# Performance work log

Hardware: AMD Instinct MI355X
Metric: run time of the kernel (lower is better)

Reference implementation:

```python
import jax, jax.numpy as jnp
import numpy as np

B, C, H, W, P, D, NH = 16, 3, 512, 512, 16, 128, 4
GH, GW = H // P, W // P
NP_ = GH * GW            # 1024 total patches
PD = C * P * P           # 768 patch dim
NV = NP_ // 4            # 256 visible tokens (mask_ratio = 0.75)
ENC_L, DEC_L = 6, 2
FF = 4 * D

def layer_norm(x, w, b, eps=1e-5):
    m = jnp.mean(x, -1, keepdims=True)
    v = jnp.mean((x - m) ** 2, -1, keepdims=True)
    return (x - m) * jax.lax.rsqrt(v + eps) * w + b

def mha(x, qkv_w, qkv_b, out_w, out_b):
    Bq, S, Dm = x.shape
    hd = Dm // NH
    q, k, v = jnp.split(x @ qkv_w.T + qkv_b, 3, axis=-1)
    sh = lambda t: t.reshape(Bq, S, NH, hd).transpose(0, 2, 1, 3)
    q, k, v = sh(q), sh(k), sh(v)
    scale = jnp.asarray(1.0 / np.sqrt(hd), x.dtype)
    att = jax.nn.softmax(jnp.einsum('bhqd,bhkd->bhqk', q, k) * scale, axis=-1)
    o = jnp.einsum('bhqk,bhkd->bhqd', att, v).transpose(0, 2, 1, 3).reshape(Bq, S, Dm)
    return o @ out_w.T + out_b

def stack(x, qkv_w, qkv_b, out_w, out_b, ln1_w, ln1_b, ff1_w, ff1_b, ff2_w, ff2_b, ln2_w, ln2_b):
    # post-norm nn.TransformerEncoderLayer, eval mode (dropout off), exact gelu
    for i in range(qkv_w.shape[0]):
        x = layer_norm(x + mha(x, qkv_w[i], qkv_b[i], out_w[i], out_b[i]), ln1_w[i], ln1_b[i])
        h = jax.nn.gelu(x @ ff1_w[i].T + ff1_b[i], approximate=False) @ ff2_w[i].T + ff2_b[i]
        x = layer_norm(x + h, ln2_w[i], ln2_b[i])
    return x

def setup_inputs():
    key = jax.random.key(0)
    ks = iter(jax.random.split(key, 64))
    f = lambda *s: jax.random.normal(next(ks), s, jnp.float32) * 0.02
    inp = {
        'x': jax.random.normal(next(ks), (B, C, H, W), jnp.float32),
        'vis_idx': jax.vmap(lambda k: jax.random.permutation(k, NP_))(jax.random.split(next(ks), B))[:, :NV].astype(jnp.int32),
        'w_patch': f(D, PD), 'b_patch': jnp.zeros((D,), jnp.float32),
        'mask_token': f(1, D), 'pos_embed': f(1, NP_, D),
        'w_recon': f(PD, D), 'b_recon': jnp.zeros((PD,), jnp.float32),
    }
    for pre, L in (('enc', ENC_L), ('dec', DEC_L)):
        inp[pre + '_qkv_w'] = f(L, 3 * D, D)
        inp[pre + '_qkv_b'] = jnp.zeros((L, 3 * D), jnp.float32)
        inp[pre + '_out_w'] = f(L, D, D)
        inp[pre + '_out_b'] = jnp.zeros((L, D), jnp.float32)
        inp[pre + '_ln1_w'] = jnp.ones((L, D), jnp.float32)
        inp[pre + '_ln1_b'] = jnp.zeros((L, D), jnp.float32)
        inp[pre + '_ff1_w'] = f(L, FF, D)
        inp[pre + '_ff1_b'] = jnp.zeros((L, FF), jnp.float32)
        inp[pre + '_ff2_w'] = f(L, D, FF)
        inp[pre + '_ff2_b'] = jnp.zeros((L, D), jnp.float32)
        inp[pre + '_ln2_w'] = jnp.ones((L, D), jnp.float32)
        inp[pre + '_ln2_b'] = jnp.zeros((L, D), jnp.float32)
    return inp

def reference(x, vis_idx, w_patch, b_patch, mask_token, pos_embed, w_recon, b_recon,
              enc_qkv_w, enc_qkv_b, enc_out_w, enc_out_b, enc_ln1_w, enc_ln1_b,
              enc_ff1_w, enc_ff1_b, enc_ff2_w, enc_ff2_b, enc_ln2_w, enc_ln2_b,
              dec_qkv_w, dec_qkv_b, dec_out_w, dec_out_b, dec_ln1_w, dec_ln1_b,
              dec_ff1_w, dec_ff1_b, dec_ff2_w, dec_ff2_b, dec_ln2_w, dec_ln2_b):
    # patchify: matches nn.Unfold(kernel=stride=P) channel-major patch layout
    patches = x.reshape(B, C, GH, P, GW, P).transpose(0, 2, 4, 1, 3, 5).reshape(B, NP_, PD)
    tok = patches @ w_patch.T + b_patch                    # [B, NP, D]
    bidx = jnp.arange(B)[:, None]
    vis = tok[bidx, vis_idx]                               # [B, NV, D] packed visible tokens
    enc = stack(vis, enc_qkv_w, enc_qkv_b, enc_out_w, enc_out_b, enc_ln1_w, enc_ln1_b,
                enc_ff1_w, enc_ff1_b, enc_ff2_w, enc_ff2_b, enc_ln2_w, enc_ln2_b)
    # mask_token everywhere, scatter encoded tokens back to their positions
    full = jnp.broadcast_to(mask_token, (B, NP_, D)).at[bidx, vis_idx].set(enc)
    full = full + pos_embed
    dec = stack(full, dec_qkv_w, dec_qkv_b, dec_out_w, dec_out_b, dec_ln1_w, dec_ln1_b,
                dec_ff1_w, dec_ff1_b, dec_ff2_w, dec_ff2_b, dec_ln2_w, dec_ln2_b)
    rec = dec @ w_recon.T + b_recon                        # [B, NP, PD]
    # unpatchify: [B,GH,GW,C,P,P] -> permute(0,3,1,4,2,5) -> [B,C,H,W]
    img = rec.reshape(B, GH, GW, C, P, P).transpose(0, 3, 1, 4, 2, 5).reshape(B, C, H, W)
    return img
```

## Files before the change

kernel.cpp:

```cpp
#include <hip/hip_runtime.h>
#include <math.h>

typedef unsigned short ushort_t;
typedef __attribute__((ext_vector_type(8))) short bf16x8;
typedef __attribute__((ext_vector_type(4))) float f32x4;
typedef __attribute__((ext_vector_type(16))) float f32x16;
typedef __attribute__((ext_vector_type(2))) unsigned uint2v;

__device__ __forceinline__ ushort_t f2bf(float f){
  union{float f; unsigned u;} v; v.f = f;
  unsigned r = v.u + 0x7FFFu + ((v.u >> 16) & 1u);
  return (ushort_t)(r >> 16);
}
__device__ __forceinline__ float bf2f(ushort_t h){
  union{unsigned u; float f;} v; v.u = ((unsigned)h) << 16; return v.f;
}
__device__ __forceinline__ float gelu_exact(float v){
  return 0.5f * v * (1.f + erff(v * 0.70710678118654752f));
}
#define GLD16(gp, lp) __builtin_amdgcn_global_load_lds( \
    (const __attribute__((address_space(1))) void*)(gp), \
    (__attribute__((address_space(3))) void*)(lp), 16, 0, 0)

static __device__ __forceinline__ f32x4 mfma16(bf16x8 a, bf16x8 b, f32x4 c){
  return __builtin_amdgcn_mfma_f32_16x16x32_bf16(a, b, c, 0, 0, 0);
}
static __device__ __forceinline__ f32x16 mfma32(bf16x8 a, bf16x8 b, f32x16 c){
  return __builtin_amdgcn_mfma_f32_32x32x16_bf16(a, b, c, 0, 0, 0);
}

template<int BT, int MI, int SRC, int EPI>
__global__ __launch_bounds__(256) void mfma_gemm(
    const ushort_t* __restrict__ A, const ushort_t* __restrict__ W,
    const float* __restrict__ bias, void* __restrict__ Cout,
    int M, int N, int K, ushort_t* __restrict__ vT, int slog, float qs)
{
  __shared__ ushort_t smem[BT*64 + BT*64];
  ushort_t* Al = smem;
  ushort_t* Wl = smem + BT*64;
  const int tid = threadIdx.x;
  const int lane = tid & 63, w = tid >> 6;
  const int wr = w >> 1, wc = w & 1;
  const int g = lane >> 4, lq = lane & 15;
  const int m0 = blockIdx.y * BT, n0 = blockIdx.x * BT;

  const f32x4 zf = {0.f, 0.f, 0.f, 0.f};
  f32x4 acc[MI][MI];
#pragma unroll
  for (int i = 0; i < MI; ++i)
#pragma unroll
    for (int j = 0; j < MI; ++j) acc[i][j] = zf;

  float bv[MI];
#pragma unroll
  for (int ni = 0; ni < MI; ++ni) bv[ni] = bias[n0 + wc*(BT/2) + ni*16 + lq];

  const int KT = K >> 6;
  for (int kt = 0; kt < KT; ++kt) {
    if (kt) __syncthreads();
    const int k0 = kt << 6;
#pragma unroll
    for (int i = 0; i < BT/32; ++i) {
      int chunk = i*256 + tid;
      int row = chunk >> 3, c = chunk & 7;
      int kk = k0 + ((c ^ (row & 7)) << 3);
      const ushort_t* src;
      if (SRC == 0) {
        src = A + (size_t)(m0 + row) * K + kk;
      } else {
        int gm = m0 + row;
        int bb = gm >> 10, pp = gm & 1023, gh = pp >> 5, gw = pp & 31;
        int ci = kk >> 8, rem = kk & 255, py = rem >> 4, px = rem & 15;
        src = A + ((size_t)((bb*3 + ci)*512 + gh*16 + py) * 512 + gw*16 + px);
      }
      GLD16(src, (char*)Al + chunk*16);
    }
#pragma unroll
    for (int i = 0; i < BT/32; ++i) {
      int chunk = i*256 + tid;
      int row = chunk >> 3, c = chunk & 7;
      int kk = k0 + ((c ^ (row & 7)) << 3);
      GLD16(W + (size_t)(n0 + row) * K + kk, (char*)Wl + chunk*16);
    }
    __syncthreads();
#pragma unroll
    for (int ks = 0; ks < 2; ++ks) {
      bf16x8 af[MI], bfr[MI];
#pragma unroll
      for (int mi = 0; mi < MI; ++mi) {
        int row = wr*(BT/2) + mi*16 + lq;
        int c = (ks*4 + g) ^ (row & 7);
        af[mi] = *(const bf16x8*)((const char*)Al + row*128 + c*16);
      }
#pragma unroll
      for (int ni = 0; ni < MI; ++ni) {
        int row = wc*(BT/2) + ni*16 + lq;
        int c = (ks*4 + g) ^ (row & 7);
        bfr[ni] = *(const bf16x8*)((const char*)Wl + row*128 + c*16);
      }
#pragma unroll
      for (int mi = 0; mi < MI; ++mi)
#pragma unroll
        for (int ni = 0; ni < MI; ++ni)
          acc[mi][ni] = mfma16(af[mi], bfr[ni], acc[mi][ni]);
    }
  }

  if (EPI == 3 && n0 >= 256) {
    const int Sm1 = (1 << slog) - 1;
#pragma unroll
    for (int mi = 0; mi < MI; ++mi) {
      int gm0 = m0 + wr*(BT/2) + mi*16 + g*4;
      int bb = gm0 >> slog, s0 = gm0 & Sm1;
#pragma unroll
      for (int ni = 0; ni < MI; ++ni) {
        int n = n0 + wc*(BT/2) + ni*16 + lq;
        int vcol = n - 256, hh = vcol >> 5, dd = vcol & 31;
        unsigned pw0 = ((unsigned)f2bf(acc[mi][ni][0] + bv[ni])) |
                       (((unsigned)f2bf(acc[mi][ni][1] + bv[ni])) << 16);
        unsigned pw1 = ((unsigned)f2bf(acc[mi][ni][2] + bv[ni])) |
                       (((unsigned)f2bf(acc[mi][ni][3] + bv[ni])) << 16);
        uint2 pk; pk.x = pw0; pk.y = pw1;
        *(uint2*)(vT + (((size_t)(bb*4 + hh)*32 + dd) << slog) + s0) = pk;
      }
    }
    return;
  }

  if (EPI == 2) {
    float* img = (float*)Cout;
#pragma unroll
    for (int mi = 0; mi < MI; ++mi) {
#pragma unroll
      for (int r = 0; r < 4; ++r) {
        int gm = m0 + wr*(BT/2) + mi*16 + g*4 + r;
        int bb = gm >> 10, pp = gm & 1023, gh = pp >> 5, gw = pp & 31;
#pragma unroll
        for (int ni = 0; ni < MI; ++ni) {
          int n = n0 + wc*(BT/2) + ni*16 + lq;
          int ci = n >> 8, rem = n & 255, py = rem >> 4, px = rem & 15;
          img[(size_t)((bb*3 + ci)*512 + gh*16 + py)*512 + gw*16 + px] =
              acc[mi][ni][r] + bv[ni];
        }
      }
    }
  } else {
    const float cs = (EPI == 3 && n0 < 128) ? qs : 1.0f;
    __syncthreads();
    constexpr int CPR = BT/8;
#pragma unroll
    for (int mi = 0; mi < MI; ++mi)
#pragma unroll
      for (int ni = 0; ni < MI; ++ni)
#pragma unroll
        for (int r = 0; r < 4; ++r) {
          int row = wr*(BT/2) + mi*16 + g*4 + r;
          int col = wc*(BT/2) + ni*16 + lq;
          float v = acc[mi][ni][r] + bv[ni];
          if (EPI == 1) v = gelu_exact(v);
          if (EPI == 3) v *= cs;
          int cc = (col >> 3) ^ (row & (CPR-1));
          smem[row*BT + cc*8 + (col & 7)] = f2bf(v);
        }
    __syncthreads();
    ushort_t* Co = (ushort_t*)Cout;
#pragma unroll
    for (int i = 0; i < BT*BT/2048; ++i) {
      int chunk = i*256 + tid;
      int row = chunk / CPR, cc = chunk % CPR;
      int c = cc ^ (row & (CPR-1));
      bf16x8 v = *(const bf16x8*)((const char*)smem + chunk*16);
      *(bf16x8*)(Co + (size_t)(m0+row)*N + n0 + c*8) = v;
    }
  }
}

template<int S, int JS>
__global__ __launch_bounds__(256) void attn32(
    const ushort_t* __restrict__ qkv, const ushort_t* __restrict__ vTg,
    ushort_t* __restrict__ o)
{
  constexpr int LDSB = (JS == 1) ? 16384 : 32768;
  __shared__ __align__(16) char smem[LDSB];
  const int tid = threadIdx.x, lane = tid & 63, w = tid >> 6;
  const int hi = lane >> 5, lq = lane & 31;
  int lin = blockIdx.x;
  int nid = (lin & 7) * 64 + (lin >> 3);
  int bx = nid & 7, bh = nid >> 3;
  int h = bh & 3, b = bh >> 2;
  const int q0 = (JS == 1) ? (bx*128 + w*32) : (bx*32);

  bf16x8 bq0 = *(const bf16x8*)(qkv + (size_t)(b*S + q0 + lq)*384 + h*32 + hi*8);
  bf16x8 bq1 = *(const bf16x8*)(qkv + (size_t)(b*S + q0 + lq)*384 + h*32 + 16 + hi*8);

  f32x16 O;
#pragma unroll
  for (int i = 0; i < 16; ++i) O[i] = 0.f;
  const f32x16 z16 = O;
  float l = 0.f;

  auto stageK = [&](char* Kb, int j0, int ci){
    int k = ci >> 2, cp = ci & 3, c = cp ^ (k & 3);
    GLD16(qkv + (size_t)(b*S + j0 + k)*384 + 128 + h*32 + c*8, Kb + ci*16);
  };
  auto stageV = [&](char* Vb, int j0, int ci){
    int d = ci >> 3, cp = ci & 7, c = cp ^ (d & 7);
    GLD16(vTg + (size_t)(bh*32 + d)*S + j0 + c*8, Vb + ci*16);
  };

  auto sm_pack = [&](const f32x16& stv, unsigned* wd){
    float p[16];
#pragma unroll
    for (int r = 0; r < 16; ++r) { p[r] = __expf(stv[r]); l += p[r]; }
#pragma unroll
    for (int i = 0; i < 8; ++i) {
      unsigned u0 = __float_as_uint(p[2*i])   + 0x8000u;
      unsigned u1 = __float_as_uint(p[2*i+1]) + 0x8000u;
      wd[i] = (u0 >> 16) | (u1 & 0xFFFF0000u);
    }
  };
  auto pvstep = [&](unsigned* wd, const char* Vb, int mt){
    uint2v s02 = __builtin_amdgcn_permlane32_swap(wd[0], wd[2], false, false);
    uint2v s13 = __builtin_amdgcn_permlane32_swap(wd[1], wd[3], false, false);
    uint2v s46 = __builtin_amdgcn_permlane32_swap(wd[4], wd[6], false, false);
    uint2v s57 = __builtin_amdgcn_permlane32_swap(wd[5], wd[7], false, false);
    union { unsigned u[4]; bf16x8 v; } pa0, pa1;
    pa0.u[0] = s02[0]; pa0.u[1] = s13[0]; pa0.u[2] = s02[1]; pa0.u[3] = s13[1];
    pa1.u[0] = s46[0]; pa1.u[1] = s57[0]; pa1.u[2] = s46[1]; pa1.u[3] = s57[1];
    int d = lq;
    bf16x8 v0 = *(const bf16x8*)(Vb + d*128 + (((mt*4 + hi)     ^ (d & 7)) << 4));
    bf16x8 v1 = *(const bf16x8*)(Vb + d*128 + (((mt*4 + 2 + hi) ^ (d & 7)) << 4));
    O = mfma32(pa0.v, v0, O);
    O = mfma32(pa1.v, v1, O);
  };
  auto computeTile = [&](const char* Kb, const char* Vb){
    const int k0 = lq, k1 = 32 + lq;
    bf16x8 a00 = *(const bf16x8*)(Kb + k0*64 + (((hi)     ^ (k0 & 3)) << 4));
    bf16x8 a01 = *(const bf16x8*)(Kb + k0*64 + (((2 + hi) ^ (k0 & 3)) << 4));
    f32x16 st0 = mfma32(a00, bq0, z16);
    st0 = mfma32(a01, bq1, st0);
    bf16x8 a10 = *(const bf16x8*)(Kb + k1*64 + (((hi)     ^ (k1 & 3)) << 4));
    bf16x8 a11 = *(const bf16x8*)(Kb + k1*64 + (((2 + hi) ^ (k1 & 3)) << 4));
    f32x16 st1 = mfma32(a10, bq0, z16);
    st1 = mfma32(a11, bq1, st1);
    unsigned wd0[8], wd1[8];
    sm_pack(st0, wd0);
    sm_pack(st1, wd1);
    pvstep(wd0, Vb, 0);
    pvstep(wd1, Vb, 1);
  };

  if (JS == 4) {
    char* Kb = smem + w*8192;
    char* Vb = Kb + 4096;
    const int j0 = w*64;
#pragma unroll
    for (int i = 0; i < 4; ++i) stageK(Kb, j0, i*64 + lane);
#pragma unroll
    for (int i = 0; i < 4; ++i) stageV(Vb, j0, i*64 + lane);
    __syncthreads();
    computeTile(Kb, Vb);
    float lw = l + __shfl_xor(l, 32);
    __syncthreads();
    float* F = (float*)smem;
#pragma unroll
    for (int r = 0; r < 16; ++r) F[(w*16 + r)*64 + lane] = O[r];
    if (hi == 0) F[4096 + w*32 + lq] = lw;
    __syncthreads();
    if (w == 0) {
      float lt = F[4096 + lq] + F[4096 + 32 + lq] + F[4096 + 64 + lq] + F[4096 + 96 + lq];
      float linv = 1.f / lt;
#pragma unroll
      for (int r = 0; r < 16; ++r) {
        float s = F[r*64 + lane] + F[(16 + r)*64 + lane] +
                  F[(32 + r)*64 + lane] + F[(48 + r)*64 + lane];
        int qr = (r & 3) + 8*(r >> 2) + 4*hi;
        float li = __shfl(linv, qr);
        o[(size_t)(b*S + q0 + qr)*128 + h*32 + lq] = f2bf(s*li);
      }
    }
  } else {
    char* K0 = smem, *V0 = smem + 4096, *K1 = smem + 8192, *V1 = smem + 12288;
    stageK(K0, 0, tid);
    stageV(V0, 0, tid);
    const int NT = S/64;
    for (int t = 0; t < NT; ++t) {
      __syncthreads();
      if (t + 1 < NT) {
        char* Kb = (t & 1) ? K0 : K1;
        char* Vb = (t & 1) ? V0 : V1;
        stageK(Kb, (t + 1)*64, tid);
        stageV(Vb, (t + 1)*64, tid);
      }
      computeTile((t & 1) ? K1 : K0, (t & 1) ? V1 : V0);
    }
    float ltot = l + __shfl_xor(l, 32);
    float linv = 1.f / ltot;
#pragma unroll
    for (int r = 0; r < 16; ++r) {
      int qr = (r & 3) + 8*(r >> 2) + 4*hi;
      float li = __shfl(linv, qr);
      o[(size_t)(b*S + q0 + qr)*128 + h*32 + lq] = f2bf(O[r]*li);
    }
  }
}

__global__ __launch_bounds__(256) void addln_bf16(
    ushort_t* __restrict__ X, const ushort_t* __restrict__ Dl,
    const float* __restrict__ wt, const float* __restrict__ bs)
{
  const int wv = threadIdx.x >> 6, lane = threadIdx.x & 63;
  const size_t row = (size_t)blockIdx.x * 4 + wv;
  ushort_t* xr = X + row*128;
  const ushort_t* dr = Dl + row*128;
  float x1 = bf2f(xr[lane])    + bf2f(dr[lane]);
  float x2 = bf2f(xr[lane+64]) + bf2f(dr[lane+64]);
  float ssum = x1 + x2;
#pragma unroll
  for (int off = 32; off; off >>= 1) ssum += __shfl_xor(ssum, off);
  float mean = ssum * 0.0078125f;
  float d1 = x1 - mean, d2 = x2 - mean;
  float v = d1*d1 + d2*d2;
#pragma unroll
  for (int off = 32; off; off >>= 1) v += __shfl_xor(v, off);
  float rs = rsqrtf(v * 0.0078125f + 1e-5f);
  xr[lane]    = f2bf(d1*rs*wt[lane]    + bs[lane]);
  xr[lane+64] = f2bf(d2*rs*wt[lane+64] + bs[lane+64]);
}

struct CastArgs {
  const float* src[11];
  ushort_t* dst[11];
  int start[11];
};
__global__ __launch_bounds__(256) void cast_all(CastArgs a, int total8){
  int i = blockIdx.x*256 + threadIdx.x;
  if (i >= total8) return;
  int s = 0;
#pragma unroll
  for (int k = 1; k < 11; ++k) if (i >= a.start[k]) s = k;
  int off = (i - a.start[s]) * 8;
  const float* sp = a.src[s] + off;
  float4 f0 = *(const float4*)sp;
  float4 f1 = *(const float4*)(sp + 4);
  bf16x8 r;
  r[0]=(short)f2bf(f0.x); r[1]=(short)f2bf(f0.y); r[2]=(short)f2bf(f0.z); r[3]=(short)f2bf(f0.w);
  r[4]=(short)f2bf(f1.x); r[5]=(short)f2bf(f1.y); r[6]=(short)f2bf(f1.z); r[7]=(short)f2bf(f1.w);
  *(bf16x8*)(a.dst[s] + off) = r;
}

__global__ __launch_bounds__(256) void gather_k(const ushort_t* __restrict__ tok,
    const int* __restrict__ vis, ushort_t* __restrict__ xe){
  int i = blockIdx.x*256 + threadIdx.x;
  int r = i >> 4, e = (i & 15)*8;
  int b = r >> 8;
  int p = vis[r];
  *(bf16x8*)(xe + (size_t)r*128 + e) = *(const bf16x8*)(tok + ((size_t)b*1024 + p)*128 + e);
}

__global__ __launch_bounds__(256) void fill_k(const float* __restrict__ mask_tok,
    const float* __restrict__ pos, ushort_t* __restrict__ full){
  int i = blockIdx.x*256 + threadIdx.x;
  int off0 = i*8;
  int d = off0 & 127;
  int p = (off0 >> 7) & 1023;
  float4 m0 = *(const float4*)(mask_tok + d);
  float4 m1 = *(const float4*)(mask_tok + d + 4);
  const float* pp = pos + (size_t)p*128 + d;
  float4 p0 = *(const float4*)pp, p1 = *(const float4*)(pp + 4);
  bf16x8 r;
  r[0]=(short)f2bf(m0.x+p0.x); r[1]=(short)f2bf(m0.y+p0.y);
  r[2]=(short)f2bf(m0.z+p0.z); r[3]=(short)f2bf(m0.w+p0.w);
  r[4]=(short)f2bf(m1.x+p1.x); r[5]=(short)f2bf(m1.y+p1.y);
  r[6]=(short)f2bf(m1.z+p1.z); r[7]=(short)f2bf(m1.w+p1.w);
  *(bf16x8*)(full + off0) = r;
}

__global__ __launch_bounds__(256) void scatter_k(const ushort_t* __restrict__ enc,
    const int* __restrict__ vis, const float* __restrict__ pos, ushort_t* __restrict__ full){
  int i = blockIdx.x*256 + threadIdx.x;
  int r = i >> 4, e = (i & 15)*8;
  int b = r >> 8;
  int p = vis[r];
  bf16x8 ev = *(const bf16x8*)(enc + (size_t)r*128 + e);
  const float* pp = pos + (size_t)p*128 + e;
  float4 p0 = *(const float4*)pp, p1 = *(const float4*)(pp + 4);
  bf16x8 out;
  out[0]=(short)f2bf(bf2f((ushort_t)ev[0]) + p0.x);
  out[1]=(short)f2bf(bf2f((ushort_t)ev[1]) + p0.y);
  out[2]=(short)f2bf(bf2f((ushort_t)ev[2]) + p0.z);
  out[3]=(short)f2bf(bf2f((ushort_t)ev[3]) + p0.w);
  out[4]=(short)f2bf(bf2f((ushort_t)ev[4]) + p1.x);
  out[5]=(short)f2bf(bf2f((ushort_t)ev[5]) + p1.y);
  out[6]=(short)f2bf(bf2f((ushort_t)ev[6]) + p1.z);
  out[7]=(short)f2bf(bf2f((ushort_t)ev[7]) + p1.w);
  *(bf16x8*)(full + ((size_t)b*1024 + p)*128 + e) = out;
}

extern "C" void kernel_launch(void* const* d_in, const int* in_sizes, int n_in,
                              void* d_out, int out_size, void* d_ws, size_t ws_size,
                              hipStream_t stream)
{
  const float* x        = (const float*)d_in[0];
  const int*   vis      = (const int*)d_in[1];
  const float* b_patch  = (const float*)d_in[3];
  const float* mask_tok = (const float*)d_in[4];
  const float* pos      = (const float*)d_in[5];
  const float* b_recon  = (const float*)d_in[7];
  float* out = (float*)d_out;
  const float QS = 0.17677669529663687f;

  ushort_t* ws    = (ushort_t*)d_ws;
  ushort_t* tok   = ws;
  ushort_t* xe    = tok  + 2097152;
  ushort_t* qkvb  = xe   + 524288;
  ushort_t* obuf  = qkvb + 8388608;
  ushort_t* tbuf  = obuf + 2097152;
  ushort_t* xbf   = tbuf + 2097152;
  ushort_t* wbf   = xbf  + 12582912;

  ushort_t* w_qkv_e = wbf;
  ushort_t* w_out_e = w_qkv_e + 294912;
  ushort_t* w_ff1_e = w_out_e + 98304;
  ushort_t* w_ff2_e = w_ff1_e + 393216;
  ushort_t* w_qkv_d = w_ff2_e + 393216;
  ushort_t* w_out_d = w_qkv_d + 98304;
  ushort_t* w_ff1_d = w_out_d + 32768;
  ushort_t* w_ff2_d = w_ff1_d + 131072;
  ushort_t* w_pat   = w_ff2_d + 131072;
  ushort_t* w_rec   = w_pat   + 98304;
  ushort_t* vT      = w_rec   + 98304;

  CastArgs ca;
  const float* srcs[11] = {x, (const float*)d_in[8], (const float*)d_in[10],
                           (const float*)d_in[14], (const float*)d_in[16],
                           (const float*)d_in[20], (const float*)d_in[22],
                           (const float*)d_in[26], (const float*)d_in[28],
                           (const float*)d_in[2], (const float*)d_in[6]};
  ushort_t* dsts[11] = {xbf, w_qkv_e, w_out_e, w_ff1_e, w_ff2_e,
                        w_qkv_d, w_out_d, w_ff1_d, w_ff2_d, w_pat, w_rec};
  int sizes[11] = {12582912, 294912, 98304, 393216, 393216,
                   98304, 32768, 131072, 131072, 98304, 98304};
  int acc8 = 0;
  for (int k = 0; k < 11; ++k){ ca.src[k]=srcs[k]; ca.dst[k]=dsts[k]; ca.start[k]=acc8; acc8 += sizes[k]/8; }
  cast_all<<<dim3((acc8 + 255)/256), 256, 0, stream>>>(ca, acc8);

  mfma_gemm<64,2,1,0><<<dim3(2,256), 256, 0, stream>>>(xbf, w_pat, b_patch, tok, 16384, 128, 768, nullptr, 0, 1.f);
  gather_k<<<dim3(256), 256, 0, stream>>>(tok, vis, xe);

  for (int L = 0; L < 6; ++L) {
    const float* qb  = (const float*)d_in[9]  + L*384;
    const float* ob  = (const float*)d_in[11] + L*128;
    const float* l1w = (const float*)d_in[12] + L*128;
    const float* l1b = (const float*)d_in[13] + L*128;
    const float* f1b = (const float*)d_in[15] + L*512;
    const float* f2b = (const float*)d_in[17] + L*128;
    const float* l2w = (const float*)d_in[18] + L*128;
    const float* l2b = (const float*)d_in[19] + L*128;
    mfma_gemm<64,2,0,3><<<dim3(6,64), 256, 0, stream>>>(xe, w_qkv_e + L*49152, qb, qkvb, 4096, 384, 128, vT, 8, QS);
    attn32<256,4><<<dim3(512), 256, 0, stream>>>(qkvb, vT, obuf);
    mfma_gemm<64,2,0,0><<<dim3(2,64), 256, 0, stream>>>(obuf, w_out_e + L*16384, ob, tbuf, 4096, 128, 128, nullptr, 0, 1.f);
    addln_bf16<<<dim3(1024), 256, 0, stream>>>(xe, tbuf, l1w, l1b);
    mfma_gemm<64,2,0,1><<<dim3(8,64), 256, 0, stream>>>(xe, w_ff1_e + L*65536, f1b, qkvb, 4096, 512, 128, nullptr, 0, 1.f);
    mfma_gemm<64,2,0,0><<<dim3(2,64), 256, 0, stream>>>(qkvb, w_ff2_e + L*65536, f2b, tbuf, 4096, 128, 512, nullptr, 0, 1.f);
    addln_bf16<<<dim3(1024), 256, 0, stream>>>(xe, tbuf, l2w, l2b);
  }

  fill_k<<<dim3(1024), 256, 0, stream>>>(mask_tok, pos, tok);
  scatter_k<<<dim3(256), 256, 0, stream>>>(xe, vis, pos, tok);

  for (int L = 0; L < 2; ++L) {
    const float* qb  = (const float*)d_in[21] + L*384;
    const float* ob  = (const float*)d_in[23] + L*128;
    const float* l1w = (const float*)d_in[24] + L*128;
    const float* l1b = (const float*)d_in[25] + L*128;
    const float* f1b = (const float*)d_in[27] + L*512;
    const float* f2b = (const float*)d_in[29] + L*128;
    const float* l2w = (const float*)d_in[30] + L*128;
    const float* l2b = (const float*)d_in[31] + L*128;
    mfma_gemm<128,4,0,3><<<dim3(3,128), 256, 0, stream>>>(tok, w_qkv_d + L*49152, qb, qkvb, 16384, 384, 128, vT, 10, QS);
    attn32<1024,1><<<dim3(512), 256, 0, stream>>>(qkvb, vT, obuf);
    mfma_gemm<64,2,0,0><<<dim3(2,256), 256, 0, stream>>>(obuf, w_out_d + L*16384, ob, tbuf, 16384, 128, 128, nullptr, 0, 1.f);
    addln_bf16<<<dim3(4096), 256, 0, stream>>>(tok, tbuf, l1w, l1b);
    mfma_gemm<128,4,0,1><<<dim3(4,128), 256, 0, stream>>>(tok, w_ff1_d + L*65536, f1b, qkvb, 16384, 512, 128, nullptr, 0, 1.f);
    mfma_gemm<64,2,0,0><<<dim3(2,256), 256, 0, stream>>>(qkvb, w_ff2_d + L*65536, f2b, tbuf, 16384, 128, 512, nullptr, 0, 1.f);
    addln_bf16<<<dim3(4096), 256, 0, stream>>>(tok, tbuf, l2w, l2b);
  }

  mfma_gemm<128,4,0,2><<<dim3(6,128), 256, 0, stream>>>(tok, w_rec, b_recon, out, 16384, 768, 128, nullptr, 0, 1.f);
}
```

Before: 396.8 us.

## Fuse out-proj with residual LayerNorm and whole FFN with residual LayerNorm

Replaces the out-projection GEMM plus separate add+LayerNorm with one gemm_ln kernel that adds bias and residual and normalizes in the epilogue, using a cross-wave reduction through shared memory. It also replaces FF1 GEMM, FF2 GEMM and add+LayerNorm with one ffn_ln kernel that keeps the 32x512 GELU hidden tile in LDS. This removes the round trips of the hidden activation and temporary buffers through global memory and cuts several launches per layer. In exchange the blocks are small (32 rows), so only 128 or 512 blocks are launched, every block reloads all of W1/W2 from global memory, there is no double buffering, and variance is computed as E[x^2]-mean^2.

New measurement: 400.1 us. About the same (+0.8%).

```diff
diff --git a/kernel.cpp b/kernel.cpp
--- a/kernel.cpp
+++ b/kernel.cpp
@@ -157,7 +157,6 @@
           int row = wr*(BT/2) + mi*16 + g*4 + r;
           int col = wc*(BT/2) + ni*16 + lq;
           float v = acc[mi][ni][r] + bv[ni];
-          if (EPI == 1) v = gelu_exact(v);
           if (EPI == 3) v *= cs;
           int cc = (col >> 3) ^ (row & (CPR-1));
           smem[row*BT + cc*8 + (col & 7)] = f2bf(v);
@@ -173,6 +172,245 @@
       *(bf16x8*)(Co + (size_t)(m0+row)*N + n0 + c*8) = v;
     }
   }
+}
+
+template<int KK>
+__global__ __launch_bounds__(256) void gemm_ln(
+    const ushort_t* __restrict__ A, const ushort_t* __restrict__ W,
+    const float* __restrict__ bias, ushort_t* __restrict__ X,
+    const float* __restrict__ lnw, const float* __restrict__ lnb)
+{
+  __shared__ __align__(16) ushort_t Al[32*64];
+  __shared__ __align__(16) ushort_t Wl[128*64];
+  __shared__ float red[2][32][4];
+  const int tid = threadIdx.x, lane = tid & 63, w = tid >> 6;
+  const int g = lane >> 4, lq = lane & 15;
+  const int m0 = blockIdx.x * 32;
+  const f32x4 zf = {0.f,0.f,0.f,0.f};
+  f32x4 acc[2][2] = {{zf,zf},{zf,zf}};
+
+#pragma unroll
+  for (int kt = 0; kt < KK/64; ++kt) {
+    if (kt) __syncthreads();
+    const int k0 = kt*64;
+    { int row = tid >> 3, c = tid & 7;
+      int kk = k0 + ((c ^ (row & 7)) << 3);
+      GLD16(A + (size_t)(m0+row)*KK + kk, (char*)Al + tid*16); }
+#pragma unroll
+    for (int i = 0; i < 4; ++i) {
+      int chunk = i*256 + tid, row = chunk >> 3, c = chunk & 7;
+      int kk = k0 + ((c ^ (row & 7)) << 3);
+      GLD16(W + (size_t)row*KK + kk, (char*)Wl + chunk*16);
+    }
+    __syncthreads();
+#pragma unroll
+    for (int ks = 0; ks < 2; ++ks) {
+      bf16x8 af[2], bfr[2];
+#pragma unroll
+      for (int mi = 0; mi < 2; ++mi) {
+        int row = mi*16 + lq, c = (ks*4 + g) ^ (row & 7);
+        af[mi] = *(const bf16x8*)((const char*)Al + row*128 + c*16);
+      }
+#pragma unroll
+      for (int ni = 0; ni < 2; ++ni) {
+        int row = w*32 + ni*16 + lq, c = (ks*4 + g) ^ (row & 7);
+        bfr[ni] = *(const bf16x8*)((const char*)Wl + row*128 + c*16);
+      }
+#pragma unroll
+      for (int mi = 0; mi < 2; ++mi)
+#pragma unroll
+        for (int ni = 0; ni < 2; ++ni)
+          acc[mi][ni] = mfma16(af[mi], bfr[ni], acc[mi][ni]);
+    }
+  }
+
+  float bv[2], lwv[2], lbv[2];
+#pragma unroll
+  for (int ni = 0; ni < 2; ++ni) {
+    int col = w*32 + ni*16 + lq;
+    bv[ni] = bias[col]; lwv[ni] = lnw[col]; lbv[ni] = lnb[col];
+  }
+  float v[2][2][4];
+#pragma unroll
+  for (int mi = 0; mi < 2; ++mi)
+#pragma unroll
+    for (int r = 0; r < 4; ++r) {
+      int row = m0 + mi*16 + g*4 + r;
+#pragma unroll
+      for (int ni = 0; ni < 2; ++ni) {
+        int col = w*32 + ni*16 + lq;
+        v[mi][ni][r] = acc[mi][ni][r] + bv[ni] + bf2f(X[(size_t)row*128 + col]);
+      }
+      float s = v[mi][0][r] + v[mi][1][r];
+      float q = v[mi][0][r]*v[mi][0][r] + v[mi][1][r]*v[mi][1][r];
+      s += __shfl_xor(s,1); s += __shfl_xor(s,2); s += __shfl_xor(s,4); s += __shfl_xor(s,8);
+      q += __shfl_xor(q,1); q += __shfl_xor(q,2); q += __shfl_xor(q,4); q += __shfl_xor(q,8);
+      if (lq == 0) { red[0][mi*16+g*4+r][w] = s; red[1][mi*16+g*4+r][w] = q; }
+    }
+  __syncthreads();
+#pragma unroll
+  for (int mi = 0; mi < 2; ++mi)
+#pragma unroll
+    for (int r = 0; r < 4; ++r) {
+      int rl = mi*16 + g*4 + r;
+      float s = red[0][rl][0]+red[0][rl][1]+red[0][rl][2]+red[0][rl][3];
+      float q = red[1][rl][0]+red[1][rl][1]+red[1][rl][2]+red[1][rl][3];
+      float mean = s * 0.0078125f;
+      float var = q * 0.0078125f - mean*mean;
+      float rstd = rsqrtf(var + 1e-5f);
+#pragma unroll
+      for (int ni = 0; ni < 2; ++ni) {
+        int col = w*32 + ni*16 + lq;
+        X[(size_t)(m0+rl)*128 + col] = f2bf((v[mi][ni][r]-mean)*rstd*lwv[ni] + lbv[ni]);
+      }
+    }
+}
+
+__global__ __launch_bounds__(256) void ffn_ln(
+    ushort_t* __restrict__ X,
+    const ushort_t* __restrict__ W1, const float* __restrict__ b1,
+    const ushort_t* __restrict__ W2, const float* __restrict__ b2,
+    const float* __restrict__ lnw, const float* __restrict__ lnb)
+{
+  __shared__ __align__(16) ushort_t Xl[2*32*64];
+  __shared__ __align__(16) ushort_t Hl[8*32*64];
+  __shared__ __align__(16) ushort_t Wl[128*64];
+  __shared__ float red[2][32][4];
+  const int tid = threadIdx.x, lane = tid & 63, w = tid >> 6;
+  const int g = lane >> 4, lq = lane & 15;
+  const int m0 = blockIdx.x * 32;
+  const f32x4 zf = {0.f,0.f,0.f,0.f};
+
+#pragma unroll
+  for (int i = 0; i < 2; ++i) {
+    int chunk = i*256 + tid;
+    int kt = chunk >> 8, r8 = chunk & 255, row = r8 >> 3, c = r8 & 7;
+    int kk = kt*64 + ((c ^ (row & 7)) << 3);
+    GLD16(X + (size_t)(m0+row)*128 + kk, (char*)Xl + chunk*16);
+  }
+
+#pragma unroll
+  for (int hp = 0; hp < 4; ++hp) {
+    f32x4 acc1[2][2] = {{zf,zf},{zf,zf}};
+#pragma unroll
+    for (int kt = 0; kt < 2; ++kt) {
+      __syncthreads();
+#pragma unroll
+      for (int i = 0; i < 4; ++i) {
+        int chunk = i*256 + tid, row = chunk >> 3, c = chunk & 7;
+        int kk = kt*64 + ((c ^ (row & 7)) << 3);
+        GLD16(W1 + (size_t)(hp*128 + row)*128 + kk, (char*)Wl + chunk*16);
+      }
+      __syncthreads();
+#pragma unroll
+      for (int ks = 0; ks < 2; ++ks) {
+        bf16x8 af[2], bfr[2];
+#pragma unroll
+        for (int mi = 0; mi < 2; ++mi) {
+          int row = mi*16 + lq, c = (ks*4 + g) ^ (row & 7);
+          af[mi] = *(const bf16x8*)((const char*)Xl + kt*4096 + row*128 + c*16);
+        }
+#pragma unroll
+        for (int ni = 0; ni < 2; ++ni) {
+          int row = w*32 + ni*16 + lq, c = (ks*4 + g) ^ (row & 7);
+          bfr[ni] = *(const bf16x8*)((const char*)Wl + row*128 + c*16);
+        }
+#pragma unroll
+        for (int mi = 0; mi < 2; ++mi)
+#pragma unroll
+          for (int ni = 0; ni < 2; ++ni)
+            acc1[mi][ni] = mfma16(af[mi], bfr[ni], acc1[mi][ni]);
+      }
+    }
+#pragma unroll
+    for (int ni = 0; ni < 2; ++ni) {
+      int hid = hp*128 + w*32 + ni*16 + lq;
+      float bb = b1[hid];
+      int hkt = hid >> 6, hc = (hid & 63) >> 3, he = hid & 7;
+#pragma unroll
+      for (int mi = 0; mi < 2; ++mi)
+#pragma unroll
+        for (int r = 0; r < 4; ++r) {
+          int mrow = mi*16 + g*4 + r;
+          float hv = gelu_exact(acc1[mi][ni][r] + bb);
+          *(ushort_t*)((char*)Hl + hkt*4096 + mrow*128 +
+                       ((hc ^ (mrow & 7)) << 4) + he*2) = f2bf(hv);
+        }
+    }
+  }
+
+  f32x4 acc2[2][2] = {{zf,zf},{zf,zf}};
+#pragma unroll
+  for (int kt = 0; kt < 8; ++kt) {
+    __syncthreads();
+#pragma unroll
+    for (int i = 0; i < 4; ++i) {
+      int chunk = i*256 + tid, row = chunk >> 3, c = chunk & 7;
+      int kk = kt*64 + ((c ^ (row & 7)) << 3);
+      GLD16(W2 + (size_t)row*512 + kk, (char*)Wl + chunk*16);
+    }
+    __syncthreads();
+#pragma unroll
+    for (int ks = 0; ks < 2; ++ks) {
+      bf16x8 af[2], bfr[2];
+#pragma unroll
+      for (int mi = 0; mi < 2; ++mi) {
+        int row = mi*16 + lq, c = (ks*4 + g) ^ (row & 7);
+        af[mi] = *(const bf16x8*)((const char*)Hl + kt*4096 + row*128 + c*16);
+      }
+#pragma unroll
+      for (int ni = 0; ni < 2; ++ni) {
+        int row = w*32 + ni*16 + lq, c = (ks*4 + g) ^ (row & 7);
+        bfr[ni] = *(const bf16x8*)((const char*)Wl + row*128 + c*16);
+      }
+#pragma unroll
+      for (int mi = 0; mi < 2; ++mi)
+#pragma unroll
+        for (int ni = 0; ni < 2; ++ni)
+          acc2[mi][ni] = mfma16(af[mi], bfr[ni], acc2[mi][ni]);
+    }
+  }
+
+  float bv[2], lwv[2], lbv[2];
+#pragma unroll
+  for (int ni = 0; ni < 2; ++ni) {
+    int col = w*32 + ni*16 + lq;
+    bv[ni] = b2[col]; lwv[ni] = lnw[col]; lbv[ni] = lnb[col];
+  }
+  float v[2][2][4];
+#pragma unroll
+  for (int mi = 0; mi < 2; ++mi)
+#pragma unroll
+    for (int r = 0; r < 4; ++r) {
+      int row = m0 + mi*16 + g*4 + r;
+#pragma unroll
+      for (int ni = 0; ni < 2; ++ni) {
+        int col = w*32 + ni*16 + lq;
+        v[mi][ni][r] = acc2[mi][ni][r] + bv[ni] + bf2f(X[(size_t)row*128 + col]);
+      }
+      float s = v[mi][0][r] + v[mi][1][r];
+      float q = v[mi][0][r]*v[mi][0][r] + v[mi][1][r]*v[mi][1][r];
+      s += __shfl_xor(s,1); s += __shfl_xor(s,2); s += __shfl_xor(s,4); s += __shfl_xor(s,8);
+      q += __shfl_xor(q,1); q += __shfl_xor(q,2); q += __shfl_xor(q,4); q += __shfl_xor(q,8);
+      if (lq == 0) { red[0][mi*16+g*4+r][w] = s; red[1][mi*16+g*4+r][w] = q; }
+    }
+  __syncthreads();
+#pragma unroll
+  for (int mi = 0; mi < 2; ++mi)
+#pragma unroll
+    for (int r = 0; r < 4; ++r) {
+      int rl = mi*16 + g*4 + r;
+      float s = red[0][rl][0]+red[0][rl][1]+red[0][rl][2]+red[0][rl][3];
+      float q = red[1][rl][0]+red[1][rl][1]+red[1][rl][2]+red[1][rl][3];
+      float mean = s * 0.0078125f;
+      float var = q * 0.0078125f - mean*mean;
+      float rstd = rsqrtf(var + 1e-5f);
+#pragma unroll
+      for (int ni = 0; ni < 2; ++ni) {
+        int col = w*32 + ni*16 + lq;
+        X[(size_t)(m0+rl)*128 + col] = f2bf((v[mi][ni][r]-mean)*rstd*lwv[ni] + lbv[ni]);
+      }
+    }
 }
 
 template<int S, int JS>
@@ -305,29 +543,6 @@
   }
 }
 
-__global__ __launch_bounds__(256) void addln_bf16(
-    ushort_t* __restrict__ X, const ushort_t* __restrict__ Dl,
-    const float* __restrict__ wt, const float* __restrict__ bs)
-{
-  const int wv = threadIdx.x >> 6, lane = threadIdx.x & 63;
-  const size_t row = (size_t)blockIdx.x * 4 + wv;
-  ushort_t* xr = X + row*128;
-  const ushort_t* dr = Dl + row*128;
-  float x1 = bf2f(xr[lane])    + bf2f(dr[lane]);
-  float x2 = bf2f(xr[lane+64]) + bf2f(dr[lane+64]);
-  float ssum = x1 + x2;
-#pragma unroll
-  for (int off = 32; off; off >>= 1) ssum += __shfl_xor(ssum, off);
-  float mean = ssum * 0.0078125f;
-  float d1 = x1 - mean, d2 = x2 - mean;
-  float v = d1*d1 + d2*d2;
-#pragma unroll
-  for (int off = 32; off; off >>= 1) v += __shfl_xor(v, off);
-  float rs = rsqrtf(v * 0.0078125f + 1e-5f);
-  xr[lane]    = f2bf(d1*rs*wt[lane]    + bs[lane]);
-  xr[lane+64] = f2bf(d2*rs*wt[lane+64] + bs[lane+64]);
-}
-
 struct CastArgs {
   const float* src[11];
   ushort_t* dst[11];
@@ -459,11 +674,8 @@
     const float* l2b = (const float*)d_in[19] + L*128;
     mfma_gemm<64,2,0,3><<<dim3(6,64), 256, 0, stream>>>(xe, w_qkv_e + L*49152, qb, qkvb, 4096, 384, 128, vT, 8, QS);
     attn32<256,4><<<dim3(512), 256, 0, stream>>>(qkvb, vT, obuf);
-    mfma_gemm<64,2,0,0><<<dim3(2,64), 256, 0, stream>>>(obuf, w_out_e + L*16384, ob, tbuf, 4096, 128, 128, nullptr, 0, 1.f);
-    addln_bf16<<<dim3(1024), 256, 0, stream>>>(xe, tbuf, l1w, l1b);
-    mfma_gemm<64,2,0,1><<<dim3(8,64), 256, 0, stream>>>(xe, w_ff1_e + L*65536, f1b, qkvb, 4096, 512, 128, nullptr, 0, 1.f);
-    mfma_gemm<64,2,0,0><<<dim3(2,64), 256, 0, stream>>>(qkvb, w_ff2_e + L*65536, f2b, tbuf, 4096, 128, 512, nullptr, 0, 1.f);
-    addln_bf16<<<dim3(1024), 256, 0, stream>>>(xe, tbuf, l2w, l2b);
+    gemm_ln<128><<<dim3(128), 256, 0, stream>>>(obuf, w_out_e + L*16384, ob, xe, l1w, l1b);
+    ffn_ln<<<dim3(128), 256, 0, stream>>>(xe, w_ff1_e + L*65536, f1b, w_ff2_e + L*65536, f2b, l2w, l2b);
   }
 
   fill_k<<<dim3(1024), 256, 0, stream>>>(mask_tok, pos, tok);
@@ -480,11 +692,8 @@
     const float* l2b = (const float*)d_in[31] + L*128;
     mfma_gemm<128,4,0,3><<<dim3(3,128), 256, 0, stream>>>(tok, w_qkv_d + L*49152, qb, qkvb, 16384, 384, 128, vT, 10, QS);
     attn32<1024,1><<<dim3(512), 256, 0, stream>>>(qkvb, vT, obuf);
-    mfma_gemm<64,2,0,0><<<dim3(2,256), 256, 0, stream>>>(obuf, w_out_d + L*16384, ob, tbuf, 16384, 128, 128, nullptr, 0, 1.f);
-    addln_bf16<<<dim3(4096), 256, 0, stream>>>(tok, tbuf, l1w, l1b);
-    mfma_gemm<128,4,0,1><<<dim3(4,128), 256, 0, stream>>>(tok, w_ff1_d + L*65536, f1b, qkvb, 16384, 512, 128, nullptr, 0, 1.f);
-    mfma_gemm<64,2,0,0><<<dim3(2,256), 256, 0, stream>>>(qkvb, w_ff2_d + L*65536, f2b, tbuf, 16384, 128, 512, nullptr, 0, 1.f);
-    addln_bf16<<<dim3(4096), 256, 0, stream>>>(tok, tbuf, l2w, l2b);
+    gemm_ln<128><<<dim3(512), 256, 0, stream>>>(obuf, w_out_d + L*16384, ob, tok, l1w, l1b);
+    ffn_ln<<<dim3(512), 256, 0, stream>>>(tok, w_ff1_d + L*65536, f1b, w_ff2_d + L*65536, f2b, l2w, l2b);
   }
 
   mfma_gemm<128,4,0,2><<<dim3(6,128), 256, 0, stream>>>(tok, w_rec, b_recon, out, 16384, 768, 128, nullptr, 0, 1.f);
```
